# Optimization experiments

Hardware: AMD Instinct MI355X
Metric: run time of the kernel (lower is better)

## Reference

```python
import jax, jax.numpy as jnp
import numpy as np

H = 32

def setup_inputs() -> dict:
    key = jax.random.key(0)
    ks = jax.random.split(key, 8)
    B, S = 256, 4096
    scale = 1.0 / np.sqrt(H)
    return {
        "lstm_outputs": jax.random.normal(ks[0], (B, S, H), dtype=jnp.float32),
        "final_hidden": jax.random.normal(ks[1], (B, H), dtype=jnp.float32),
        "Wq": jax.random.uniform(ks[2], (H, H), jnp.float32, -scale, scale),
        "bq": jax.random.uniform(ks[3], (H,), jnp.float32, -scale, scale),
        "Wk": jax.random.uniform(ks[4], (H, H), jnp.float32, -scale, scale),
        "bk": jax.random.uniform(ks[5], (H,), jnp.float32, -scale, scale),
        "Wv": jax.random.uniform(ks[6], (H, 1), jnp.float32, -scale, scale),
        "bv": jax.random.uniform(ks[7], (1,), jnp.float32, -scale, scale),
    }

def reference(lstm_outputs, final_hidden, Wq, bq, Wk, bk, Wv, bv):
    # keys: [B,S,H], query: [B,H]
    keys = jnp.einsum('bsh,hd->bsd', lstm_outputs, Wk) + bk
    query = final_hidden @ Wq + bq
    tanhed = jnp.tanh(query[:, None, :] + keys)            # [B,S,H]
    scores = jnp.einsum('bsh,h->bs', tanhed, Wv[:, 0]) + bv[0]  # [B,S]
    att_weights = jax.nn.softmax(scores, axis=-1)          # [B,S]
    context = jnp.einsum('bs,bsh->bh', att_weights, keys)  # [B,H]
    return context, att_weights
```

## Files before the change

kernel.cpp:

```cpp
#include <hip/hip_runtime.h>
#include <math.h>

#define HD 32
#define BB 256
#define SS 4096
#define CHUNK 512
#define NC (SS / CHUNK)
#define BLK 256
#define PART_STRIDE 34

typedef float vf32 __attribute__((ext_vector_type(32)));

__device__ __forceinline__ float tanh_fast(float x) {
  float e = __builtin_amdgcn_exp2f(x * 2.8853900817779268f);
  return 1.0f - 2.0f * __builtin_amdgcn_rcpf(e + 1.0f);
}
__device__ __forceinline__ float exp_fast(float x) {
  return __builtin_amdgcn_exp2f(x * 1.4426950408889634f);
}

__global__ void __launch_bounds__(BLK, 3) bahdanau_p1(
    const float* __restrict__ lstm, const float* __restrict__ fh,
    const float* __restrict__ Wq, const float* __restrict__ bq,
    const float* __restrict__ Wk, const float* __restrict__ bk,
    const float* __restrict__ Wv, const float* __restrict__ bv,
    float* __restrict__ scores_out, float* __restrict__ partials) {
  __shared__ float sQ[HD];
  __shared__ float sRedM[BLK / 64];
  __shared__ float sRedL[BLK / 64];
  __shared__ float sRedC[BLK / 64][HD];

  const int tid = threadIdx.x;
  const int b = blockIdx.x / NC;
  const int chunk = blockIdx.x % NC;
  const int base = chunk * CHUNK;

  const int sA = base + tid;
  const int sB = sA + BLK;
  const float* rowA = lstm + ((size_t)b * SS + sA) * HD;
  const float* rowB = rowA + (size_t)BLK * HD;

  vf32 xA, xB;
#pragma unroll
  for (int q = 0; q < 8; q++) {
    float4 t = ((const float4*)rowA)[q];
    xA[4 * q + 0] = t.x; xA[4 * q + 1] = t.y;
    xA[4 * q + 2] = t.z; xA[4 * q + 3] = t.w;
  }
#pragma unroll
  for (int q = 0; q < 8; q++) {
    float4 t = ((const float4*)rowB)[q];
    xB[4 * q + 0] = t.x; xB[4 * q + 1] = t.y;
    xB[4 * q + 2] = t.z; xB[4 * q + 3] = t.w;
  }

  if (tid < HD) {
    float acc = bq[tid];
    const float* fhb = fh + b * HD;
#pragma unroll
    for (int j = 0; j < HD; j++) acc += fhb[j] * Wq[j * HD + tid];
    sQ[tid] = acc;
  }
  __syncthreads();

  vf32 kA, kB;
#pragma unroll
  for (int h = 0; h < HD; h++) {
    float bkh = bk[h];
    kA[h] = bkh; kB[h] = bkh;
  }
#pragma unroll
  for (int j = 0; j < HD; j++) {
    const float xa = xA[j];
    const float xb = xB[j];
#pragma unroll
    for (int h = 0; h < HD; h++) {
      const float w = Wk[j * HD + h];
      kA[h] = fmaf(xa, w, kA[h]);
      kB[h] = fmaf(xb, w, kB[h]);
    }
  }

  const float bv0 = bv[0];
  float scA = bv0, scB = bv0;
#pragma unroll
  for (int h = 0; h < HD; h++) {
    const float qh = sQ[h];
    const float wv = Wv[h];
    scA = fmaf(tanh_fast(qh + kA[h]), wv, scA);
    scB = fmaf(tanh_fast(qh + kB[h]), wv, scB);
  }
  scores_out[(size_t)b * SS + sA] = scA;
  scores_out[(size_t)b * SS + sB] = scB;

  const int wid = tid >> 6, lane = tid & 63;
  float m = fmaxf(scA, scB);
#pragma unroll
  for (int off = 32; off >= 1; off >>= 1) m = fmaxf(m, __shfl_xor(m, off, 64));
  if (lane == 0) sRedM[wid] = m;
  __syncthreads();
  m = fmaxf(fmaxf(sRedM[0], sRedM[1]), fmaxf(sRedM[2], sRedM[3]));

  const float eA = exp_fast(scA - m);
  const float eB = exp_fast(scB - m);
  float l = eA + eB;
#pragma unroll
  for (int off = 32; off >= 1; off >>= 1) l += __shfl_xor(l, off, 64);
  if (lane == 0) sRedL[wid] = l;

#pragma unroll
  for (int h = 0; h < HD; h++) {
    float v = fmaf(eA, kA[h], eB * kB[h]);
#pragma unroll
    for (int off = 32; off >= 1; off >>= 1) v += __shfl_xor(v, off, 64);
    if (lane == 0) sRedC[wid][h] = v;
  }
  __syncthreads();

  if (tid < HD) {
    float c = sRedC[0][tid] + sRedC[1][tid] + sRedC[2][tid] + sRedC[3][tid];
    float* p = partials + (size_t)(b * NC + chunk) * PART_STRIDE;
    p[2 + tid] = c;
    if (tid == 0) {
      p[0] = m;
      p[1] = sRedL[0] + sRedL[1] + sRedL[2] + sRedL[3];
    }
  }
}

__global__ void __launch_bounds__(BLK) bahdanau_p2(
    const float* __restrict__ partials, float* __restrict__ ctx_out,
    float* __restrict__ scores) {
  const int b = blockIdx.x / NC;
  const int chunk = blockIdx.x % NC;
  const int tid = threadIdx.x;

  float m = -1e30f;
#pragma unroll
  for (int c = 0; c < NC; c++)
    m = fmaxf(m, partials[(size_t)(b * NC + c) * PART_STRIDE]);
  float L = 0.f;
  float al[NC];
#pragma unroll
  for (int c = 0; c < NC; c++) {
    const float* p = partials + (size_t)(b * NC + c) * PART_STRIDE;
    float a = exp_fast(p[0] - m);
    al[c] = a;
    L = fmaf(a, p[1], L);
  }
  const float invL = __builtin_amdgcn_rcpf(L);

  if (chunk == 0 && tid < HD) {
    float c = 0.f;
#pragma unroll
    for (int cc = 0; cc < NC; cc++)
      c += al[cc] * partials[(size_t)(b * NC + cc) * PART_STRIDE + 2 + tid];
    ctx_out[b * HD + tid] = c * invL;
  }

  float2* srow = (float2*)(scores + (size_t)b * SS + chunk * CHUNK);
  float2 s = srow[tid];
  s.x = exp_fast(s.x - m) * invL;
  s.y = exp_fast(s.y - m) * invL;
  srow[tid] = s;
}

extern "C" void kernel_launch(void* const* d_in, const int* in_sizes, int n_in,
                              void* d_out, int out_size, void* d_ws,
                              size_t ws_size, hipStream_t stream) {
  const float* lstm = (const float*)d_in[0];
  const float* fh   = (const float*)d_in[1];
  const float* Wq   = (const float*)d_in[2];
  const float* bq   = (const float*)d_in[3];
  const float* Wk   = (const float*)d_in[4];
  const float* bk   = (const float*)d_in[5];
  const float* Wv   = (const float*)d_in[6];
  const float* bv   = (const float*)d_in[7];

  float* out = (float*)d_out;
  float* ctx_out = out;
  float* scores = out + BB * HD;
  float* partials = (float*)d_ws;

  bahdanau_p1<<<BB * NC, BLK, 0, stream>>>(lstm, fh, Wq, bq, Wk, bk, Wv, bv,
                                           scores, partials);
  bahdanau_p2<<<BB * NC, BLK, 0, stream>>>(partials, ctx_out, scores);
}
```

Baseline: 239.2 us.

## Drop softmax max pass, stream rows, use recursive-halving butterfly context reduction

Scores are exponentiated directly without subtracting a block maximum. This removes the max reduction, one block barrier, and the rescaling work in the second kernel, whose softmax pass now only multiplies by 1/L. Each thread now processes its two rows one after the other instead of holding both at once, and the launch-bounds occupancy hint rises from 3 to 5. The 32 separate full-wave shuffle reductions for the context are replaced by a recursive-halving butterfly that leaves one context component per lane. Skipping the max relies on scores staying small (tanh output times small Wv), so larger weights could overflow the exponential.

```diff
diff --git a/kernel.cpp b/kernel.cpp
--- a/kernel.cpp
+++ b/kernel.cpp
@@ -7,9 +7,8 @@
 #define CHUNK 512
 #define NC (SS / CHUNK)
 #define BLK 256
-#define PART_STRIDE 34
-
-typedef float vf32 __attribute__((ext_vector_type(32)));
+#define NSTEP 2
+#define PART_STRIDE 33
 
 __device__ __forceinline__ float tanh_fast(float x) {
   float e = __builtin_amdgcn_exp2f(x * 2.8853900817779268f);
@@ -19,40 +18,25 @@
   return __builtin_amdgcn_exp2f(x * 1.4426950408889634f);
 }
 
-__global__ void __launch_bounds__(BLK, 3) bahdanau_p1(
+__device__ __forceinline__ int bitrev5(int lane) {
+  return ((lane & 1) << 4) | ((lane & 2) << 2) | (lane & 4) |
+         ((lane & 8) >> 2) | ((lane & 16) >> 4);
+}
+
+__global__ void __launch_bounds__(BLK, 5) bahdanau_p1(
     const float* __restrict__ lstm, const float* __restrict__ fh,
     const float* __restrict__ Wq, const float* __restrict__ bq,
     const float* __restrict__ Wk, const float* __restrict__ bk,
     const float* __restrict__ Wv, const float* __restrict__ bv,
     float* __restrict__ scores_out, float* __restrict__ partials) {
   __shared__ float sQ[HD];
-  __shared__ float sRedM[BLK / 64];
   __shared__ float sRedL[BLK / 64];
   __shared__ float sRedC[BLK / 64][HD];
 
   const int tid = threadIdx.x;
   const int b = blockIdx.x / NC;
   const int chunk = blockIdx.x % NC;
-  const int base = chunk * CHUNK;
-
-  const int sA = base + tid;
-  const int sB = sA + BLK;
-  const float* rowA = lstm + ((size_t)b * SS + sA) * HD;
-  const float* rowB = rowA + (size_t)BLK * HD;
-
-  vf32 xA, xB;
-#pragma unroll
-  for (int q = 0; q < 8; q++) {
-    float4 t = ((const float4*)rowA)[q];
-    xA[4 * q + 0] = t.x; xA[4 * q + 1] = t.y;
-    xA[4 * q + 2] = t.z; xA[4 * q + 3] = t.w;
-  }
-#pragma unroll
-  for (int q = 0; q < 8; q++) {
-    float4 t = ((const float4*)rowB)[q];
-    xB[4 * q + 0] = t.x; xB[4 * q + 1] = t.y;
-    xB[4 * q + 2] = t.z; xB[4 * q + 3] = t.w;
-  }
+  const int lane = tid & 63, wid = tid >> 6;
 
   if (tid < HD) {
     float acc = bq[tid];
@@ -63,68 +47,76 @@
   }
   __syncthreads();
 
-  vf32 kA, kB;
+  const float bv0 = bv[0];
+  float lAcc = 0.f;
+  float ctxLane = 0.f;
+
 #pragma unroll
-  for (int h = 0; h < HD; h++) {
-    float bkh = bk[h];
-    kA[h] = bkh; kB[h] = bkh;
-  }
+  for (int st = 0; st < NSTEP; st++) {
+    const int s = chunk * CHUNK + st * BLK + tid;
+    const float* row = lstm + ((size_t)b * SS + s) * HD;
+
+    float x[HD];
 #pragma unroll
-  for (int j = 0; j < HD; j++) {
-    const float xa = xA[j];
-    const float xb = xB[j];
+    for (int q = 0; q < 8; q++) {
+      float4 t = ((const float4*)row)[q];
+      x[4 * q + 0] = t.x; x[4 * q + 1] = t.y;
+      x[4 * q + 2] = t.z; x[4 * q + 3] = t.w;
+    }
+
+    float k[HD];
 #pragma unroll
-    for (int h = 0; h < HD; h++) {
-      const float w = Wk[j * HD + h];
-      kA[h] = fmaf(xa, w, kA[h]);
-      kB[h] = fmaf(xb, w, kB[h]);
+    for (int h = 0; h < HD; h++) k[h] = bk[h];
+#pragma unroll
+    for (int j = 0; j < HD; j++) {
+      const float xj = x[j];
+#pragma unroll
+      for (int h = 0; h < HD; h++) k[h] = fmaf(xj, Wk[j * HD + h], k[h]);
     }
+
+    float sc = bv0;
+#pragma unroll
+    for (int h = 0; h < HD; h++)
+      sc = fmaf(tanh_fast(sQ[h] + k[h]), Wv[h], sc);
+    const float e = exp_fast(sc);
+    scores_out[(size_t)b * SS + s] = e;
+    lAcc += e;
+
+    float arr[HD];
+#pragma unroll
+    for (int h = 0; h < HD; h++) arr[h] = e * k[h];
+    int n = HD;
+#pragma unroll
+    for (int lv = 0; lv < 5; lv++) {
+      const int half = n >> 1;
+      const bool up = (lane >> lv) & 1;
+#pragma unroll
+      for (int i = 0; i < 16; i++) {
+        if (i < half) {
+          float send = up ? arr[i] : arr[i + half];
+          float keep = up ? arr[i + half] : arr[i];
+          float recv = __shfl_xor(send, 1 << lv, 64);
+          arr[i] = keep + recv;
+        }
+      }
+      n = half;
+    }
+    float v = arr[0];
+    v += __shfl_xor(v, 32, 64);
+    ctxLane += v;
   }
 
-  const float bv0 = bv[0];
-  float scA = bv0, scB = bv0;
 #pragma unroll
-  for (int h = 0; h < HD; h++) {
-    const float qh = sQ[h];
-    const float wv = Wv[h];
-    scA = fmaf(tanh_fast(qh + kA[h]), wv, scA);
-    scB = fmaf(tanh_fast(qh + kB[h]), wv, scB);
-  }
-  scores_out[(size_t)b * SS + sA] = scA;
-  scores_out[(size_t)b * SS + sB] = scB;
-
-  const int wid = tid >> 6, lane = tid & 63;
-  float m = fmaxf(scA, scB);
-#pragma unroll
-  for (int off = 32; off >= 1; off >>= 1) m = fmaxf(m, __shfl_xor(m, off, 64));
-  if (lane == 0) sRedM[wid] = m;
-  __syncthreads();
-  m = fmaxf(fmaxf(sRedM[0], sRedM[1]), fmaxf(sRedM[2], sRedM[3]));
-
-  const float eA = exp_fast(scA - m);
-  const float eB = exp_fast(scB - m);
-  float l = eA + eB;
-#pragma unroll
-  for (int off = 32; off >= 1; off >>= 1) l += __shfl_xor(l, off, 64);
-  if (lane == 0) sRedL[wid] = l;
-
-#pragma unroll
-  for (int h = 0; h < HD; h++) {
-    float v = fmaf(eA, kA[h], eB * kB[h]);
-#pragma unroll
-    for (int off = 32; off >= 1; off >>= 1) v += __shfl_xor(v, off, 64);
-    if (lane == 0) sRedC[wid][h] = v;
-  }
+  for (int off = 32; off >= 1; off >>= 1) lAcc += __shfl_xor(lAcc, off, 64);
+  if (lane == 0) sRedL[wid] = lAcc;
+  if (lane < HD) sRedC[wid][bitrev5(lane)] = ctxLane;
   __syncthreads();
 
   if (tid < HD) {
     float c = sRedC[0][tid] + sRedC[1][tid] + sRedC[2][tid] + sRedC[3][tid];
     float* p = partials + (size_t)(b * NC + chunk) * PART_STRIDE;
-    p[2 + tid] = c;
-    if (tid == 0) {
-      p[0] = m;
-      p[1] = sRedL[0] + sRedL[1] + sRedL[2] + sRedL[3];
-    }
+    p[1 + tid] = c;
+    if (tid == 0) p[0] = sRedL[0] + sRedL[1] + sRedL[2] + sRedL[3];
   }
 }
 
@@ -135,33 +127,24 @@
   const int chunk = blockIdx.x % NC;
   const int tid = threadIdx.x;
 
-  float m = -1e30f;
+  float L = 0.f;
 #pragma unroll
   for (int c = 0; c < NC; c++)
-    m = fmaxf(m, partials[(size_t)(b * NC + c) * PART_STRIDE]);
-  float L = 0.f;
-  float al[NC];
-#pragma unroll
-  for (int c = 0; c < NC; c++) {
-    const float* p = partials + (size_t)(b * NC + c) * PART_STRIDE;
-    float a = exp_fast(p[0] - m);
-    al[c] = a;
-    L = fmaf(a, p[1], L);
-  }
+    L += partials[(size_t)(b * NC + c) * PART_STRIDE];
   const float invL = __builtin_amdgcn_rcpf(L);
 
   if (chunk == 0 && tid < HD) {
     float c = 0.f;
 #pragma unroll
     for (int cc = 0; cc < NC; cc++)
-      c += al[cc] * partials[(size_t)(b * NC + cc) * PART_STRIDE + 2 + tid];
+      c += partials[(size_t)(b * NC + cc) * PART_STRIDE + 1 + tid];
     ctx_out[b * HD + tid] = c * invL;
   }
 
   float2* srow = (float2*)(scores + (size_t)b * SS + chunk * CHUNK);
   float2 s = srow[tid];
-  s.x = exp_fast(s.x - m) * invL;
-  s.y = exp_fast(s.y - m) * invL;
+  s.x *= invL;
+  s.y *= invL;
   srow[tid] = s;
 }
 
```

Result: slower. 287.5 us (+20.2%).
